# Kernel optimization log

Measured on AMD Instinct MI355X. Metric: run time of the kernel, lower is better.

The kernel has to match this reference:

```python
import jax, jax.numpy as jnp
import numpy as np

IN_SIZE = 64
RES = 1024
B = 16
T = 2048
ALPHA = 0.5
SPECTRAL_RADIUS = 0.9


def setup_inputs() -> dict:
    key = jax.random.key(0)
    ks = jax.random.split(key, 8)
    # W_hh scaled so spectral radius ~ SPECTRAL_RADIUS (circular law: |eig|max ~ sqrt(R)*std)
    scale_hh = SPECTRAL_RADIUS / np.sqrt(RES)
    return {
        "x": jax.random.normal(ks[0], (B, T, IN_SIZE), dtype=jnp.float32),
        "W_in0": jax.random.normal(ks[1], (IN_SIZE, RES), dtype=jnp.float32) * 0.5,
        "W_hh0": jax.random.normal(ks[2], (RES, RES), dtype=jnp.float32) * scale_hh,
        "b0": jax.random.normal(ks[3], (1, RES), dtype=jnp.float32) * 0.5,
        "W_in1": jax.random.normal(ks[4], (RES, RES), dtype=jnp.float32) * 0.1,
        "W_hh1": jax.random.normal(ks[5], (RES, RES), dtype=jnp.float32) * scale_hh,
        "b1": jax.random.normal(ks[6], (1, RES), dtype=jnp.float32) * 0.5,
        "readout": jax.random.normal(ks[7], (2 * RES, IN_SIZE), dtype=jnp.float32) * 0.02,
    }


def _reservoir_layer(xs, W_in, W_hh, b, alpha):
    # xs: [T, B, F] time-major; sequential leaky-integrator scan over T
    h0 = jnp.zeros((xs.shape[1], W_hh.shape[0]), dtype=xs.dtype)

    def step(h, x_i):
        h = (1.0 - alpha) * h + alpha * jnp.tanh(x_i @ W_in + h @ W_hh + b)
        return h, h

    _, states = jax.lax.scan(step, h0, xs)
    return states  # [T, B, R]


def reference(x, W_in0, W_hh0, b0, W_in1, W_hh1, b1, readout):
    xt = jnp.transpose(x, (1, 0, 2))  # [T, B, in]
    s0 = _reservoir_layer(xt, W_in0, W_hh0, b0, ALPHA)  # [T, B, R]
    s1 = _reservoir_layer(s0, W_in1, W_hh1, b1, ALPHA)  # [T, B, R]
    h = jnp.concatenate([s0, s1], axis=-1)  # [T, B, 2R]
    out = h @ readout  # [T, B, in]
    return jnp.transpose(out, (1, 0, 2))  # [B, T, in]
```

## Files before the change

### kernel.cpp

```cpp
#include <hip/hip_runtime.h>
#include <math.h>

#define ESN_B 16
#define ESN_T 2048
#define ESN_R 1024
#define ESN_IN 64
#define NBR (ESN_B * ESN_R)

#define OFF_WT_HH0 0
#define OFF_WT_IN1 (1024 * 1024)
#define OFF_WT_HH1 (2 * 1024 * 1024)
#define OFF_WT_IN0 (3 * 1024 * 1024)
#define OFF_RT     (OFF_WT_IN0 + 1024 * 64)
#define OFF_S0G    (OFF_RT + 64 * 2048)
#define OFF_S1G    (OFF_S0G + 2 * NBR)
#define OFF_FLAGS  (OFF_S1G + 2 * NBR)

__global__ void __launch_bounds__(256) transpose_k(const float* __restrict__ src,
                                                   float* __restrict__ dst,
                                                   int rows, int cols) {
  __shared__ float tile[32][33];
  int bx = blockIdx.x * 32, by = blockIdx.y * 32;
  int tx = threadIdx.x, ty = threadIdx.y;
  #pragma unroll
  for (int i = ty; i < 32; i += 8) {
    int r = by + i, c = bx + tx;
    if (r < rows && c < cols) tile[i][tx] = src[(size_t)r * cols + c];
  }
  __syncthreads();
  #pragma unroll
  for (int i = ty; i < 32; i += 8) {
    int c = bx + i, r = by + tx;
    if (c < cols && r < rows) dst[(size_t)c * rows + r] = tile[tx][i];
  }
}

__device__ __forceinline__ float fast_tanh(float v) {
  float a = fabsf(v);
  float e = __expf(-2.0f * a);
  float t = __fdividef(1.0f - e, 1.0f + e);
  return copysignf(t, v);
}

__device__ __forceinline__ float dot4(float4 a, float4 b, float acc) {
  acc = fmaf(a.x, b.x, acc);
  acc = fmaf(a.y, b.y, acc);
  acc = fmaf(a.z, b.z, acc);
  acc = fmaf(a.w, b.w, acc);
  return acc;
}

__device__ __forceinline__ float wave_red64(float v) {
  #pragma unroll
  for (int off = 32; off > 0; off >>= 1) v += __shfl_xor(v, off, 64);
  return v;
}

__device__ __forceinline__ float reduce4(float a0, float a1, float a2, float a3,
                                         bool lb0, bool lb1) {
  float uA = lb0 ? a0 : a1, kA = lb0 ? a1 : a0;
  float A = kA + __shfl_xor(uA, 1, 64);
  float uB = lb0 ? a2 : a3, kB = lb0 ? a3 : a2;
  float B = kB + __shfl_xor(uB, 1, 64);
  float uC = lb1 ? A : B, kC = lb1 ? B : A;
  float C = kC + __shfl_xor(uC, 2, 64);
  C += __shfl_xor(C, 4, 64);
  C += __shfl_xor(C, 8, 64);
  C += __shfl_xor(C, 16, 64);
  C += __shfl_xor(C, 32, 64);
  return C;
}

__device__ __forceinline__ void llc_store_f32(float* p, float v) {
  asm volatile("global_store_dword %0, %1, off sc1" :: "v"(p), "v"(v) : "memory");
}
__device__ __forceinline__ void llc_store_u32(unsigned* p, unsigned v) {
  asm volatile("global_store_dword %0, %1, off sc1" :: "v"(p), "v"(v) : "memory");
}
__device__ __forceinline__ unsigned llc_load_u32(const unsigned* p) {
  unsigned f;
  asm volatile("global_load_dword %0, %1, off sc1\n\ts_waitcnt vmcnt(0)"
               : "=v"(f) : "v"(p) : "memory");
  return f;
}
__device__ __forceinline__ void vmcnt0() {
  asm volatile("s_waitcnt vmcnt(0)" ::: "memory");
}

__global__ void __launch_bounds__(256, 1) esn_scan_kernel(
    const float* __restrict__ x,
    const float* __restrict__ b0,
    const float* __restrict__ b1,
    float* __restrict__ wsf,
    float* __restrict__ out) {
  __shared__ float s0l[2][4][1024];
  __shared__ float s1l[4][1024];
  extern __shared__ float dyn_pad[];
  if (blockIdx.x == 0x7fffffffu) dyn_pad[0] = 1.0f;

  const float* wtHH0 = wsf + OFF_WT_HH0;
  const float* wtIN1 = wsf + OFF_WT_IN1;
  const float* wtHH1 = wsf + OFF_WT_HH1;
  const float* wtIN0 = wsf + OFF_WT_IN0;
  const float* rt    = wsf + OFF_RT;
  float* s0g = wsf + OFF_S0G;
  float* s1g = wsf + OFF_S1G;
  unsigned* flags = (unsigned*)(wsf + OFF_FLAGS);

  const int tid = threadIdx.x;
  const int l = tid & 63;
  const int w = tid >> 6;
  const int bid = blockIdx.x;
  const int g = bid >> 6;
  const int bg = bid & 63;
  const int batch0 = g * 4;
  const int c0 = (bg * 4 + w) * 4;
  const int wg = bg * 4 + w;
  const int rbl = wg >> 6;
  const int rb = batch0 + rbl;
  const int roc = wg & 63;
  unsigned* gflags = flags + g * 64;
  const bool lb0 = (l & 1) != 0;
  const bool lb1 = (l & 2) != 0;

  float4 whh0[4][4], win1[4][4], whh1[4][4], rdt[8];
  float win0v[4];
  #pragma unroll
  for (int cc = 0; cc < 4; ++cc) {
    const float* p0 = wtHH0 + (size_t)(c0 + cc) * ESN_R + l * 4;
    const float* p1 = wtIN1 + (size_t)(c0 + cc) * ESN_R + l * 4;
    const float* p2 = wtHH1 + (size_t)(c0 + cc) * ESN_R + l * 4;
    #pragma unroll
    for (int q = 0; q < 4; ++q) {
      whh0[cc][q] = *(const float4*)(p0 + q * 256);
      win1[cc][q] = *(const float4*)(p1 + q * 256);
      whh1[cc][q] = *(const float4*)(p2 + q * 256);
    }
    win0v[cc] = wtIN0[(size_t)(c0 + cc) * ESN_IN + l];
  }
  #pragma unroll
  for (int q = 0; q < 8; ++q)
    rdt[q] = *(const float4*)(rt + (size_t)roc * 2048 + q * 256 + l * 4);
  const float b0sel = b0[c0 + (l & 3)];
  const float b1sel = b1[c0 + (l & 3)];

  for (int r = 0; r < ESN_T + 2; ++r) {
    const int slot = r & 1, oslot = slot ^ 1;
    const bool doL0 = (r < ESN_T);
    const bool doL1 = (r >= 1 && r <= ESN_T);

    float xv[4];
    if (doL0) {
      #pragma unroll
      for (int bb = 0; bb < 4; ++bb)
        xv[bb] = x[((size_t)(batch0 + bb) * ESN_T + r) * ESN_IN + l];
    }

    if (r > 0) {
      if (w == 0) {
        while (!__all(llc_load_u32(&gflags[l]) >= (unsigned)r)) {}
      }
      __syncthreads();
    }

    {
      const float* gs0 = s0g + oslot * NBR + batch0 * ESN_R + tid * 4;
      const float* gs1 = s1g + oslot * NBR + batch0 * ESN_R + tid * 4;
      float4 t0, t1, t2, t3, u0, u1, u2, u3;
      asm volatile(
          "global_load_dwordx4 %0, %8, off sc1\n\t"
          "global_load_dwordx4 %1, %9, off sc1\n\t"
          "global_load_dwordx4 %2, %10, off sc1\n\t"
          "global_load_dwordx4 %3, %11, off sc1\n\t"
          "global_load_dwordx4 %4, %12, off sc1\n\t"
          "global_load_dwordx4 %5, %13, off sc1\n\t"
          "global_load_dwordx4 %6, %14, off sc1\n\t"
          "global_load_dwordx4 %7, %15, off sc1\n\t"
          "s_waitcnt vmcnt(0)"
          : "=&v"(t0), "=&v"(t1), "=&v"(t2), "=&v"(t3),
            "=&v"(u0), "=&v"(u1), "=&v"(u2), "=&v"(u3)
          : "v"(gs0), "v"(gs0 + 1024), "v"(gs0 + 2048), "v"(gs0 + 3072),
            "v"(gs1), "v"(gs1 + 1024), "v"(gs1 + 2048), "v"(gs1 + 3072)
          : "memory");
      float* d0 = &s0l[slot][0][0] + tid * 4;
      float* d1 = &s1l[0][0] + tid * 4;
      *(float4*)(d0)        = t0;
      *(float4*)(d0 + 1024) = t1;
      *(float4*)(d0 + 2048) = t2;
      *(float4*)(d0 + 3072) = t3;
      *(float4*)(d1)        = u0;
      *(float4*)(d1 + 1024) = u1;
      *(float4*)(d1 + 2048) = u2;
      *(float4*)(d1 + 3072) = u3;
    }
    __syncthreads();

    for (int bb = 0; bb < 4; ++bb) {
      float4 h0f[4];
      #pragma unroll
      for (int q = 0; q < 4; ++q)
        h0f[q] = *(const float4*)(&s0l[slot][bb][q * 256 + l * 4]);

      if (doL0) {
        float a0 = xv[bb] * win0v[0], a1 = xv[bb] * win0v[1];
        float a2 = xv[bb] * win0v[2], a3 = xv[bb] * win0v[3];
        #pragma unroll
        for (int q = 0; q < 4; ++q) {
          a0 = dot4(whh0[0][q], h0f[q], a0);
          a1 = dot4(whh0[1][q], h0f[q], a1);
          a2 = dot4(whh0[2][q], h0f[q], a2);
          a3 = dot4(whh0[3][q], h0f[q], a3);
        }
        float C = reduce4(a0, a1, a2, a3, lb0, lb1);
        if (l < 4) {
          float prev = s0l[slot][bb][c0 + l];
          float nv = 0.5f * prev + 0.5f * fast_tanh(C + b0sel);
          llc_store_f32(&s0g[slot * NBR + (batch0 + bb) * ESN_R + c0 + l], nv);
        }
      }
      if (doL1) {
        float4 h1f[4];
        #pragma unroll
        for (int q = 0; q < 4; ++q)
          h1f[q] = *(const float4*)(&s1l[bb][q * 256 + l * 4]);
        float a0 = 0.f, a1 = 0.f, a2 = 0.f, a3 = 0.f;
        #pragma unroll
        for (int q = 0; q < 4; ++q) {
          a0 = dot4(win1[0][q], h0f[q], a0); a0 = dot4(whh1[0][q], h1f[q], a0);
          a1 = dot4(win1[1][q], h0f[q], a1); a1 = dot4(whh1[1][q], h1f[q], a1);
          a2 = dot4(win1[2][q], h0f[q], a2); a2 = dot4(whh1[2][q], h1f[q], a2);
          a3 = dot4(win1[3][q], h0f[q], a3); a3 = dot4(whh1[3][q], h1f[q], a3);
        }
        float C = reduce4(a0, a1, a2, a3, lb0, lb1);
        if (l < 4) {
          float prev = s1l[bb][c0 + l];
          float nv = 0.5f * prev + 0.5f * fast_tanh(C + b1sel);
          llc_store_f32(&s1g[slot * NBR + (batch0 + bb) * ESN_R + c0 + l], nv);
        }
      }
    }

    vmcnt0();
    __syncthreads();
    if (tid == 0) llc_store_u32(&gflags[bg], (unsigned)(r + 1));

    if (r >= 2) {
      float a = 0.f;
      #pragma unroll
      for (int q = 0; q < 4; ++q)
        a = dot4(rdt[q], *(const float4*)(&s0l[oslot][rbl][q * 256 + l * 4]), a);
      #pragma unroll
      for (int q = 0; q < 4; ++q)
        a = dot4(rdt[q + 4], *(const float4*)(&s1l[rbl][q * 256 + l * 4]), a);
      a = wave_red64(a);
      if (l == 0) out[((size_t)rb * ESN_T + (r - 2)) * ESN_IN + roc] = a;
    }
  }
}

extern "C" void kernel_launch(void* const* d_in, const int* in_sizes, int n_in,
                              void* d_out, int out_size, void* d_ws, size_t ws_size,
                              hipStream_t stream) {
  (void)in_sizes; (void)n_in; (void)out_size; (void)ws_size;
  const float* x     = (const float*)d_in[0];
  const float* w_in0 = (const float*)d_in[1];
  const float* w_hh0 = (const float*)d_in[2];
  const float* b0    = (const float*)d_in[3];
  const float* w_in1 = (const float*)d_in[4];
  const float* w_hh1 = (const float*)d_in[5];
  const float* b1    = (const float*)d_in[6];
  const float* rdo   = (const float*)d_in[7];
  float* out = (float*)d_out;
  float* wsf = (float*)d_ws;

  dim3 tb(32, 8);
  transpose_k<<<dim3(32, 32), tb, 0, stream>>>(w_hh0, wsf + OFF_WT_HH0, 1024, 1024);
  transpose_k<<<dim3(32, 32), tb, 0, stream>>>(w_in1, wsf + OFF_WT_IN1, 1024, 1024);
  transpose_k<<<dim3(32, 32), tb, 0, stream>>>(w_hh1, wsf + OFF_WT_HH1, 1024, 1024);
  transpose_k<<<dim3(32, 2),  tb, 0, stream>>>(w_in0, wsf + OFF_WT_IN0, 64, 1024);
  transpose_k<<<dim3(2, 64),  tb, 0, stream>>>(rdo,   wsf + OFF_RT, 2048, 64);

  hipMemsetAsync(wsf + OFF_S0G + NBR, 0, NBR * sizeof(float), stream);
  hipMemsetAsync(wsf + OFF_S1G, 0, NBR * sizeof(float), stream);
  hipMemsetAsync(wsf + OFF_FLAGS, 0, 4 * 64 * sizeof(unsigned), stream);

  esn_scan_kernel<<<dim3(256), dim3(256), 40960, stream>>>(x, b0, b1, wsf, out);
}
```

Measured before the change: 13.80 ms.

## Use per-wave completion flags and drop the block barrier before signaling

Each wave now publishes its own progress flag after its stores drain, so the __syncthreads before the per-block flag store is gone. The spinning wave polls four flags per lane with one dwordx4 load, keeping a single poll covering all 256 wave flags per group. The weight and state arrays are also unrolled into named scalars so they reliably stay in registers. The aim is to shorten the per-timestep critical path of the cross-block barrier, at the cost of four times as many flag words to poll.

```diff
diff --git a/kernel.cpp b/kernel.cpp
--- a/kernel.cpp
+++ b/kernel.cpp
@@ -77,9 +77,9 @@
 __device__ __forceinline__ void llc_store_u32(unsigned* p, unsigned v) {
   asm volatile("global_store_dword %0, %1, off sc1" :: "v"(p), "v"(v) : "memory");
 }
-__device__ __forceinline__ unsigned llc_load_u32(const unsigned* p) {
-  unsigned f;
-  asm volatile("global_load_dword %0, %1, off sc1\n\ts_waitcnt vmcnt(0)"
+__device__ __forceinline__ uint4 llc_load_u32x4(const unsigned* p) {
+  uint4 f;
+  asm volatile("global_load_dwordx4 %0, %1, off sc1\n\ts_waitcnt vmcnt(0)"
                : "=v"(f) : "v"(p) : "memory");
   return f;
 }
@@ -119,28 +119,44 @@
   const int rbl = wg >> 6;
   const int rb = batch0 + rbl;
   const int roc = wg & 63;
-  unsigned* gflags = flags + g * 64;
+  unsigned* gflags = flags + g * 256;
   const bool lb0 = (l & 1) != 0;
   const bool lb1 = (l & 2) != 0;
 
-  float4 whh0[4][4], win1[4][4], whh1[4][4], rdt[8];
-  float win0v[4];
-  #pragma unroll
-  for (int cc = 0; cc < 4; ++cc) {
-    const float* p0 = wtHH0 + (size_t)(c0 + cc) * ESN_R + l * 4;
-    const float* p1 = wtIN1 + (size_t)(c0 + cc) * ESN_R + l * 4;
-    const float* p2 = wtHH1 + (size_t)(c0 + cc) * ESN_R + l * 4;
-    #pragma unroll
-    for (int q = 0; q < 4; ++q) {
-      whh0[cc][q] = *(const float4*)(p0 + q * 256);
-      win1[cc][q] = *(const float4*)(p1 + q * 256);
-      whh1[cc][q] = *(const float4*)(p2 + q * 256);
-    }
-    win0v[cc] = wtIN0[(size_t)(c0 + cc) * ESN_IN + l];
-  }
-  #pragma unroll
-  for (int q = 0; q < 8; ++q)
-    rdt[q] = *(const float4*)(rt + (size_t)roc * 2048 + q * 256 + l * 4);
+  float4 wA0_0, wA0_1, wA0_2, wA0_3, wA1_0, wA1_1, wA1_2, wA1_3;
+  float4 wA2_0, wA2_1, wA2_2, wA2_3, wA3_0, wA3_1, wA3_2, wA3_3;
+  float4 wB0_0, wB0_1, wB0_2, wB0_3, wB1_0, wB1_1, wB1_2, wB1_3;
+  float4 wB2_0, wB2_1, wB2_2, wB2_3, wB3_0, wB3_1, wB3_2, wB3_3;
+  float4 wC0_0, wC0_1, wC0_2, wC0_3, wC1_0, wC1_1, wC1_2, wC1_3;
+  float4 wC2_0, wC2_1, wC2_2, wC2_3, wC3_0, wC3_1, wC3_2, wC3_3;
+  float4 rd0, rd1, rd2, rd3, rd4, rd5, rd6, rd7;
+  float wI0, wI1, wI2, wI3;
+
+#define LOADW(cc) { \
+    const float* pA = wtHH0 + (size_t)(c0 + cc) * ESN_R + l * 4; \
+    const float* pB = wtIN1 + (size_t)(c0 + cc) * ESN_R + l * 4; \
+    const float* pC = wtHH1 + (size_t)(c0 + cc) * ESN_R + l * 4; \
+    wA##cc##_0 = *(const float4*)(pA);       wA##cc##_1 = *(const float4*)(pA + 256); \
+    wA##cc##_2 = *(const float4*)(pA + 512); wA##cc##_3 = *(const float4*)(pA + 768); \
+    wB##cc##_0 = *(const float4*)(pB);       wB##cc##_1 = *(const float4*)(pB + 256); \
+    wB##cc##_2 = *(const float4*)(pB + 512); wB##cc##_3 = *(const float4*)(pB + 768); \
+    wC##cc##_0 = *(const float4*)(pC);       wC##cc##_1 = *(const float4*)(pC + 256); \
+    wC##cc##_2 = *(const float4*)(pC + 512); wC##cc##_3 = *(const float4*)(pC + 768); \
+  }
+  LOADW(0) LOADW(1) LOADW(2) LOADW(3)
+#undef LOADW
+
+  {
+    const float* pr = rt + (size_t)roc * 2048 + l * 4;
+    rd0 = *(const float4*)(pr);        rd1 = *(const float4*)(pr + 256);
+    rd2 = *(const float4*)(pr + 512);  rd3 = *(const float4*)(pr + 768);
+    rd4 = *(const float4*)(pr + 1024); rd5 = *(const float4*)(pr + 1280);
+    rd6 = *(const float4*)(pr + 1536); rd7 = *(const float4*)(pr + 1792);
+  }
+  wI0 = wtIN0[(size_t)(c0 + 0) * ESN_IN + l];
+  wI1 = wtIN0[(size_t)(c0 + 1) * ESN_IN + l];
+  wI2 = wtIN0[(size_t)(c0 + 2) * ESN_IN + l];
+  wI3 = wtIN0[(size_t)(c0 + 3) * ESN_IN + l];
   const float b0sel = b0[c0 + (l & 3)];
   const float b1sel = b1[c0 + (l & 3)];
 
@@ -149,16 +165,22 @@
     const bool doL0 = (r < ESN_T);
     const bool doL1 = (r >= 1 && r <= ESN_T);
 
-    float xv[4];
+    float xv0 = 0.f, xv1 = 0.f, xv2 = 0.f, xv3 = 0.f;
     if (doL0) {
-      #pragma unroll
-      for (int bb = 0; bb < 4; ++bb)
-        xv[bb] = x[((size_t)(batch0 + bb) * ESN_T + r) * ESN_IN + l];
+      xv0 = x[((size_t)(batch0 + 0) * ESN_T + r) * ESN_IN + l];
+      xv1 = x[((size_t)(batch0 + 1) * ESN_T + r) * ESN_IN + l];
+      xv2 = x[((size_t)(batch0 + 2) * ESN_T + r) * ESN_IN + l];
+      xv3 = x[((size_t)(batch0 + 3) * ESN_T + r) * ESN_IN + l];
     }
 
     if (r > 0) {
       if (w == 0) {
-        while (!__all(llc_load_u32(&gflags[l]) >= (unsigned)r)) {}
+        for (;;) {
+          uint4 f = llc_load_u32x4(&gflags[l * 4]);
+          bool ok = f.x >= (unsigned)r && f.y >= (unsigned)r &&
+                    f.z >= (unsigned)r && f.w >= (unsigned)r;
+          if (__all(ok)) break;
+        }
       }
       __syncthreads();
     }
@@ -196,21 +218,20 @@
     __syncthreads();
 
     for (int bb = 0; bb < 4; ++bb) {
-      float4 h0f[4];
-      #pragma unroll
-      for (int q = 0; q < 4; ++q)
-        h0f[q] = *(const float4*)(&s0l[slot][bb][q * 256 + l * 4]);
+      const float* hp = &s0l[slot][bb][l * 4];
+      float4 h0x = *(const float4*)(hp);
+      float4 h1x = *(const float4*)(hp + 256);
+      float4 h2x = *(const float4*)(hp + 512);
+      float4 h3x = *(const float4*)(hp + 768);
+      float xb = (bb == 0) ? xv0 : (bb == 1) ? xv1 : (bb == 2) ? xv2 : xv3;
 
       if (doL0) {
-        float a0 = xv[bb] * win0v[0], a1 = xv[bb] * win0v[1];
-        float a2 = xv[bb] * win0v[2], a3 = xv[bb] * win0v[3];
-        #pragma unroll
-        for (int q = 0; q < 4; ++q) {
-          a0 = dot4(whh0[0][q], h0f[q], a0);
-          a1 = dot4(whh0[1][q], h0f[q], a1);
-          a2 = dot4(whh0[2][q], h0f[q], a2);
-          a3 = dot4(whh0[3][q], h0f[q], a3);
-        }
+        float a0 = xb * wI0, a1 = xb * wI1, a2 = xb * wI2, a3 = xb * wI3;
+#define DOT_A(cc, acc) \
+        acc = dot4(wA##cc##_0, h0x, acc); acc = dot4(wA##cc##_1, h1x, acc); \
+        acc = dot4(wA##cc##_2, h2x, acc); acc = dot4(wA##cc##_3, h3x, acc);
+        DOT_A(0, a0) DOT_A(1, a1) DOT_A(2, a2) DOT_A(3, a3)
+#undef DOT_A
         float C = reduce4(a0, a1, a2, a3, lb0, lb1);
         if (l < 4) {
           float prev = s0l[slot][bb][c0 + l];
@@ -219,18 +240,19 @@
         }
       }
       if (doL1) {
-        float4 h1f[4];
-        #pragma unroll
-        for (int q = 0; q < 4; ++q)
-          h1f[q] = *(const float4*)(&s1l[bb][q * 256 + l * 4]);
+        const float* gp = &s1l[bb][l * 4];
+        float4 g0x = *(const float4*)(gp);
+        float4 g1x = *(const float4*)(gp + 256);
+        float4 g2x = *(const float4*)(gp + 512);
+        float4 g3x = *(const float4*)(gp + 768);
         float a0 = 0.f, a1 = 0.f, a2 = 0.f, a3 = 0.f;
-        #pragma unroll
-        for (int q = 0; q < 4; ++q) {
-          a0 = dot4(win1[0][q], h0f[q], a0); a0 = dot4(whh1[0][q], h1f[q], a0);
-          a1 = dot4(win1[1][q], h0f[q], a1); a1 = dot4(whh1[1][q], h1f[q], a1);
-          a2 = dot4(win1[2][q], h0f[q], a2); a2 = dot4(whh1[2][q], h1f[q], a2);
-          a3 = dot4(win1[3][q], h0f[q], a3); a3 = dot4(whh1[3][q], h1f[q], a3);
-        }
+#define DOT_BC(cc, acc) \
+        acc = dot4(wB##cc##_0, h0x, acc); acc = dot4(wB##cc##_1, h1x, acc); \
+        acc = dot4(wB##cc##_2, h2x, acc); acc = dot4(wB##cc##_3, h3x, acc); \
+        acc = dot4(wC##cc##_0, g0x, acc); acc = dot4(wC##cc##_1, g1x, acc); \
+        acc = dot4(wC##cc##_2, g2x, acc); acc = dot4(wC##cc##_3, g3x, acc);
+        DOT_BC(0, a0) DOT_BC(1, a1) DOT_BC(2, a2) DOT_BC(3, a3)
+#undef DOT_BC
         float C = reduce4(a0, a1, a2, a3, lb0, lb1);
         if (l < 4) {
           float prev = s1l[bb][c0 + l];
@@ -241,17 +263,20 @@
     }
 
     vmcnt0();
-    __syncthreads();
-    if (tid == 0) llc_store_u32(&gflags[bg], (unsigned)(r + 1));
+    if (l == 0) llc_store_u32(&gflags[bg * 4 + w], (unsigned)(r + 1));
 
     if (r >= 2) {
+      const float* sp = &s0l[oslot][rbl][l * 4];
+      const float* tp = &s1l[rbl][l * 4];
       float a = 0.f;
-      #pragma unroll
-      for (int q = 0; q < 4; ++q)
-        a = dot4(rdt[q], *(const float4*)(&s0l[oslot][rbl][q * 256 + l * 4]), a);
-      #pragma unroll
-      for (int q = 0; q < 4; ++q)
-        a = dot4(rdt[q + 4], *(const float4*)(&s1l[rbl][q * 256 + l * 4]), a);
+      a = dot4(rd0, *(const float4*)(sp), a);
+      a = dot4(rd1, *(const float4*)(sp + 256), a);
+      a = dot4(rd2, *(const float4*)(sp + 512), a);
+      a = dot4(rd3, *(const float4*)(sp + 768), a);
+      a = dot4(rd4, *(const float4*)(tp), a);
+      a = dot4(rd5, *(const float4*)(tp + 256), a);
+      a = dot4(rd6, *(const float4*)(tp + 512), a);
+      a = dot4(rd7, *(const float4*)(tp + 768), a);
       a = wave_red64(a);
       if (l == 0) out[((size_t)rb * ESN_T + (r - 2)) * ESN_IN + roc] = a;
     }
@@ -282,7 +307,7 @@
 
   hipMemsetAsync(wsf + OFF_S0G + NBR, 0, NBR * sizeof(float), stream);
   hipMemsetAsync(wsf + OFF_S1G, 0, NBR * sizeof(float), stream);
-  hipMemsetAsync(wsf + OFF_FLAGS, 0, 4 * 64 * sizeof(unsigned), stream);
+  hipMemsetAsync(wsf + OFF_FLAGS, 0, 4 * 256 * sizeof(unsigned), stream);
 
   esn_scan_kernel<<<dim3(256), dim3(256), 40960, stream>>>(x, b0, b1, wsf, out);
 }
```

Result: no change. 13.88 ms (+0.6%).
